# Optimization experiments

Hardware: AMD Instinct MI355X
Metric: run time of the kernel (lower is better)

Reference implementation:

```python
import jax, jax.numpy as jnp
import numpy as np

NUM_GRAPHS = 256


def _mean_aggregate(h, src, dst, num_nodes):
    # DGL copy_src + mean reduce: dst node gets mean of src-node features over in-edges.
    summed = jax.ops.segment_sum(h[src], dst, num_segments=num_nodes)  # [N, F]
    deg = jax.ops.segment_sum(jnp.ones((src.shape[0],), h.dtype), dst, num_segments=num_nodes)
    return summed / jnp.maximum(deg, 1.0)[:, None]


def setup_inputs() -> dict:
    key = jax.random.key(0)
    ks = jax.random.split(key, 10)
    N, E, D_IN, H1, H2, OUT = 50000, 800000, 128, 256, 128, 1
    s = lambda fan: 1.0 / np.sqrt(fan)
    return {
        "h": jax.random.normal(ks[0], (N, D_IN), jnp.float32),
        "src": jax.random.randint(ks[1], (E,), 0, N),
        "dst": jax.random.randint(ks[2], (E,), 0, N),
        "graph_ids": jnp.sort(jax.random.randint(ks[3], (N,), 0, NUM_GRAPHS)),
        "W1": jax.random.normal(ks[4], (D_IN, H1), jnp.float32) * s(D_IN),
        "b1": jnp.zeros((H1,), jnp.float32),
        "W2": jax.random.normal(ks[5], (H1, H1), jnp.float32) * s(H1),
        "b2": jnp.zeros((H1,), jnp.float32),
        "Wr1": jax.random.normal(ks[6], (H1, H2), jnp.float32) * s(H1),
        "br1": jnp.zeros((H2,), jnp.float32),
        "Wr2": jax.random.normal(ks[7], (H2, OUT), jnp.float32) * s(H2),
        "br2": jnp.zeros((OUT,), jnp.float32),
    }


def reference(h, src, dst, graph_ids, W1, b1, W2, b2, Wr1, br1, Wr2, br2):
    N = h.shape[0]
    # GCN layer 1: mean-aggregate then linear+ReLU
    h = _mean_aggregate(h, src, dst, N)
    h = jax.nn.relu(h @ W1 + b1)
    # GCN layer 2
    h = _mean_aggregate(h, src, dst, N)
    h = jax.nn.relu(h @ W2 + b2)
    # dgl.mean_nodes readout: per-graph mean of node features
    gsum = jax.ops.segment_sum(h, graph_ids, num_segments=NUM_GRAPHS)  # [G, H1]
    gcnt = jax.ops.segment_sum(jnp.ones((N,), h.dtype), graph_ids, num_segments=NUM_GRAPHS)
    hg = gsum / jnp.maximum(gcnt, 1.0)[:, None]
    hidden = hg @ Wr1 + br1
    return hidden @ Wr2 + br2  # [G, 1]
```

## Files before the change

kernel.cpp:

```cpp
#include <hip/hip_runtime.h>


#define NUM_GRAPHS 256

#define CNT_B0 0
#define CNT_NB 1024
#define CST_B0 (CNT_B0 + CNT_NB)
#define CST_NB 512
#define GST_B0 (CST_B0 + CST_NB)
#define GST_NB 64
#define WT1_B0 (GST_B0 + GST_NB)
#define WT1_NB 16
#define WT2_B0 (WT1_B0 + WT1_NB)
#define WT2_NB 32
#define MISC_NB (WT2_B0 + WT2_NB)

typedef __attribute__((ext_vector_type(8))) short bf16x8;
typedef __attribute__((ext_vector_type(4))) float f32x4;

__device__ inline unsigned short f2bf(float f) {
    unsigned u = __float_as_uint(f);
    return (unsigned short)((u + 0x7fff + ((u >> 16) & 1)) >> 16);
}
__device__ inline float bflo(unsigned u) { return __uint_as_float(u << 16); }
__device__ inline float bfhi(unsigned u) { return __uint_as_float(u & 0xffff0000u); }


__launch_bounds__(256)
__global__ void misc_kernel(const int* __restrict__ dst, const int* __restrict__ gids,
                            const float* __restrict__ h,
                            const float* __restrict__ W1, const float* __restrict__ W2,
                            int* __restrict__ cnt, unsigned short* __restrict__ rank,
                            int* __restrict__ gstart,
                            unsigned short* __restrict__ hb,
                            unsigned short* __restrict__ Wt1, unsigned short* __restrict__ Wt2,
                            int N, int E) {
    int b = blockIdx.x, tid = threadIdx.x;
    if (b < CST_B0) {
        int lid = (b - CNT_B0) * 256 + tid;
        for (int e = lid; e < E; e += CNT_NB * 256) {
            int d = __builtin_nontemporal_load(&dst[e]);
            int r = atomicAdd(&cnt[d], 1);
            __builtin_nontemporal_store((unsigned short)r, &rank[e]);
        }
    } else if (b < GST_B0) {
        int lid = (b - CST_B0) * 256 + tid;
        int total4 = N * 32;
        for (int i = lid; i < total4; i += CST_NB * 256) {
            float4 v = *(const float4*)(h + (size_t)i * 4);
            ushort4 o;
            o.x = f2bf(v.x); o.y = f2bf(v.y); o.z = f2bf(v.z); o.w = f2bf(v.w);
            *(ushort4*)(hb + (size_t)i * 4) = o;
        }
    } else if (b < WT1_B0) {
        int lid = (b - GST_B0) * 256 + tid;
        for (int n = lid; n < N; n += GST_NB * 256) {
            int g = gids[n];
            int gp = (n == 0) ? -1 : gids[n - 1];
            for (int x = gp + 1; x <= g; ++x) gstart[x] = n;
            if (n == N - 1)
                for (int x = g + 1; x <= NUM_GRAPHS; ++x) gstart[x] = N;
        }
    } else if (b < WT2_B0) {
        int lid = (b - WT1_B0) * 256 + tid;
        for (int i = lid; i < 256 * 128; i += WT1_NB * 256)
            Wt1[i] = f2bf(W1[(size_t)(i & 127) * 256 + (i >> 7)]);
    } else {
        int lid = (b - WT2_B0) * 256 + tid;
        for (int i = lid; i < 256 * 256; i += WT2_NB * 256)
            Wt2[i] = f2bf(W2[(size_t)(i & 255) * 256 + (i >> 8)]);
    }
}


__global__ void scan_kernel(const int* __restrict__ cnt, int* __restrict__ offs,
                            int* __restrict__ pval, int* __restrict__ pflag,
                            int N, int E) {
    __shared__ int wsum[16];
    __shared__ int sbase;
    int tid = threadIdx.x;
    int lane = tid & 63;
    int wid = tid >> 6;
    int b = blockIdx.x;
    int i = b * 1024 + tid;
    int v = (i < N) ? cnt[i] : 0;
    int x = v;
    #pragma unroll
    for (int d = 1; d < 64; d <<= 1) {
        int y = __shfl_up(x, d, 64);
        if (lane >= d) x += y;
    }
    if (lane == 63) wsum[wid] = x;
    __syncthreads();
    if (wid == 0) {
        int s = (lane < 16) ? wsum[lane] : 0;
        #pragma unroll
        for (int d = 1; d < 16; d <<= 1) {
            int y = __shfl_up(s, d, 64);
            if (lane >= d) s += y;
        }
        if (lane < 16) wsum[lane] = s;
    }
    __syncthreads();
    int wbase = (wid > 0) ? wsum[wid - 1] : 0;
    int ex = wbase + x - v;

    if (tid == 1023)
        atomicExch(&pval[b], (wbase + x) | 0x40000000);
    if (wid == 0) {
        int sum = 0;
        if (lane < b) {
            int pv;
            do { pv = atomicAdd(&pval[lane], 0); } while (!(pv & 0x40000000));
            sum = pv & 0x3fffffff;
        }
        #pragma unroll
        for (int d = 32; d > 0; d >>= 1) sum += __shfl_xor(sum, d, 64);
        if (lane == 0) sbase = sum;
    }
    __syncthreads();
    if (i < N) offs[i] = sbase + ex;
    if (b == 0 && tid == 0) offs[N] = E;
    (void)pflag;
}


__global__ void scatter_kernel(const int* __restrict__ src, const int* __restrict__ dst,
                               const int* __restrict__ offs,
                               const unsigned short* __restrict__ rank,
                               unsigned short* __restrict__ eidx, int E) {
    int e = blockIdx.x * blockDim.x + threadIdx.x;
    if (e < E) {
        int d = __builtin_nontemporal_load(&dst[e]);
        unsigned short r = __builtin_nontemporal_load(&rank[e]);
        int s = __builtin_nontemporal_load(&src[e]);
        eidx[offs[d] + (int)r] = (unsigned short)s;
    }
}


template <int D>
__global__ void agg_mean_bf16_kernel(const unsigned short* __restrict__ feat,
                                     const int* __restrict__ offs,
                                     const unsigned short* __restrict__ eidx,
                                     unsigned short* __restrict__ out, int N) {
    constexpr int VPL = D / 64;
    int wave = blockIdx.x * (blockDim.x >> 6) + (threadIdx.x >> 6);
    int lane = threadIdx.x & 63;
    if (wave >= N) return;
    int beg = offs[wave], end = offs[wave + 1];
    float acc[VPL];
    #pragma unroll
    for (int i = 0; i < VPL; ++i) acc[i] = 0.0f;

    for (int base = beg; base < end; base += 64) {
        int nchunk = end - base;
        if (nchunk > 64) nchunk = 64;
        int myIdx = (lane < nchunk) ? (int)eidx[base + lane] : 0;

        int j = 0;
        for (; j + 8 <= nchunk; j += 8) {
            int s[8];
            #pragma unroll
            for (int u = 0; u < 8; ++u) s[u] = __shfl(myIdx, j + u, 64);
            if constexpr (VPL == 2) {
                unsigned v[8];
                #pragma unroll
                for (int u = 0; u < 8; ++u)
                    v[u] = *(const unsigned*)(feat + (size_t)s[u] * D + lane * 2);
                #pragma unroll
                for (int u = 0; u < 8; ++u) { acc[0] += bflo(v[u]); acc[1] += bfhi(v[u]); }
            } else {
                uint2 v[8];
                #pragma unroll
                for (int u = 0; u < 8; ++u)
                    v[u] = *(const uint2*)(feat + (size_t)s[u] * D + lane * 4);
                #pragma unroll
                for (int u = 0; u < 8; ++u) {
                    acc[0] += bflo(v[u].x); acc[1] += bfhi(v[u].x);
                    acc[2] += bflo(v[u].y); acc[3] += bfhi(v[u].y);
                }
            }
        }
        for (; j < nchunk; ++j) {
            int s = __shfl(myIdx, j, 64);
            if constexpr (VPL == 2) {
                unsigned v = *(const unsigned*)(feat + (size_t)s * D + lane * 2);
                acc[0] += bflo(v); acc[1] += bfhi(v);
            } else {
                uint2 v = *(const uint2*)(feat + (size_t)s * D + lane * 4);
                acc[0] += bflo(v.x); acc[1] += bfhi(v.x);
                acc[2] += bflo(v.y); acc[3] += bfhi(v.y);
            }
        }
    }

    int deg = end - beg;
    float invd = 1.0f / (float)(deg > 0 ? deg : 1);
    unsigned short* orow = out + (size_t)wave * D + lane * VPL;
    if constexpr (VPL == 2) {
        ushort2 o; o.x = f2bf(acc[0] * invd); o.y = f2bf(acc[1] * invd);
        *(ushort2*)orow = o;
    } else {
        ushort4 o;
        o.x = f2bf(acc[0] * invd); o.y = f2bf(acc[1] * invd);
        o.z = f2bf(acc[2] * invd); o.w = f2bf(acc[3] * invd);
        *(ushort4*)orow = o;
    }
}


template <int K, int MODE>
__launch_bounds__(256)
__global__ void gemm_mfma_kernel(const unsigned short* __restrict__ A,
                                 const unsigned short* __restrict__ Wt,
                                 const float* __restrict__ bias,
                                 unsigned short* __restrict__ Cb,
                                 const int* __restrict__ gids,
                                 float* __restrict__ gsum,
                                 int N) {
    constexpr int LDS = 40;
    __shared__ unsigned short As[64 * LDS];
    __shared__ unsigned short Bs[256 * LDS];

    int tid = threadIdx.x;
    int wave = tid >> 6;
    int lane = tid & 63;
    int m = lane & 15;
    int q = lane >> 4;
    int rowBase = blockIdx.x * 64;

    f32x4 acc[4][4] = {};

    for (int kc = 0; kc < K; kc += 32) {
        {
            int r = tid >> 2;
            int seg = tid & 3;
            int gr = rowBase + r;
            uint4 v = make_uint4(0, 0, 0, 0);
            if (gr < N) v = *(const uint4*)(A + (size_t)gr * K + kc + seg * 8);
            *(uint4*)&As[r * LDS + seg * 8] = v;
        }
        #pragma unroll
        for (int it = 0; it < 4; ++it) {
            int n = (tid >> 2) + it * 64;
            int seg = tid & 3;
            uint4 v = *(const uint4*)(Wt + (size_t)n * K + kc + seg * 8);
            *(uint4*)&Bs[n * LDS + seg * 8] = v;
        }
        __syncthreads();

        bf16x8 af[4], bfr[4];
        #pragma unroll
        for (int r = 0; r < 4; ++r)
            af[r] = *(const bf16x8*)&As[(r * 16 + m) * LDS + q * 8];
        #pragma unroll
        for (int c = 0; c < 4; ++c)
            bfr[c] = *(const bf16x8*)&Bs[(wave * 64 + c * 16 + m) * LDS + q * 8];
        #pragma unroll
        for (int r = 0; r < 4; ++r)
            #pragma unroll
            for (int c = 0; c < 4; ++c)
                acc[r][c] = __builtin_amdgcn_mfma_f32_16x16x32_bf16(af[r], bfr[c], acc[r][c], 0, 0, 0);
        __syncthreads();
    }

    if constexpr (MODE == 0) {
        #pragma unroll
        for (int c = 0; c < 4; ++c) {
            int col = wave * 64 + c * 16 + m;
            float bv = bias[col];
            #pragma unroll
            for (int r = 0; r < 4; ++r) {
                #pragma unroll
                for (int reg = 0; reg < 4; ++reg) {
                    int grow = rowBase + r * 16 + q * 4 + reg;
                    if (grow < N)
                        Cb[(size_t)grow * 256 + col] = f2bf(fmaxf(acc[r][c][reg] + bv, 0.0f));
                }
            }
        }
    } else {
        int* sgid = (int*)As;
        if (tid < 64) {
            int gr = rowBase + tid;
            sgid[tid] = (gr < N) ? gids[gr] : 0x7fffffff;
        }
        __syncthreads();
        int lastValid = N - 1 - rowBase;
        if (lastValid > 63) lastValid = 63;
        int gmin = sgid[0];
        int gmax = sgid[lastValid];
        #pragma unroll
        for (int c = 0; c < 4; ++c) {
            int col = wave * 64 + c * 16 + m;
            float bv = bias[col];
            for (int g = gmin; g <= gmax; ++g) {
                float p = 0.0f;
                #pragma unroll
                for (int r = 0; r < 4; ++r) {
                    #pragma unroll
                    for (int reg = 0; reg < 4; ++reg) {
                        int lr = r * 16 + q * 4 + reg;
                        if (sgid[lr] == g)
                            p += fmaxf(acc[r][c][reg] + bv, 0.0f);
                    }
                }
                p += __shfl_xor(p, 16, 64);
                p += __shfl_xor(p, 32, 64);
                if (q == 0 && p != 0.0f)
                    atomicAdd(&gsum[g * 256 + col], p);
            }
        }
    }
}


__global__ void final_kernel(const float* __restrict__ gsum, const int* __restrict__ gstart,
                             const float* __restrict__ Wr1, const float* __restrict__ br1,
                             const float* __restrict__ Wr2, const float* __restrict__ br2,
                             float* __restrict__ out) {
    __shared__ float part[512];
    __shared__ float ws2[2];
    int g = blockIdx.x;
    int t = threadIdx.x;
    int j = t & 127;
    int kq = t >> 7;
    int c = gstart[g + 1] - gstart[g];
    float invc = 1.0f / (float)(c > 0 ? c : 1);
    const float* gs = gsum + g * 256;
    float acc = 0.0f;
    #pragma unroll 8
    for (int k = kq * 64; k < kq * 64 + 64; ++k)
        acc += gs[k] * Wr1[k * 128 + j];
    part[t] = acc;
    __syncthreads();
    if (t < 128) {
        float s = part[j] + part[128 + j] + part[256 + j] + part[384 + j];
        float p = (s * invc + br1[j]) * Wr2[j];
        #pragma unroll
        for (int d = 32; d > 0; d >>= 1) p += __shfl_down(p, d, 64);
        if ((t & 63) == 0) ws2[t >> 6] = p;
    }
    __syncthreads();
    if (t == 0) out[g] = ws2[0] + ws2[1] + br2[0];
}


extern "C" void kernel_launch(void* const* d_in, const int* in_sizes, int n_in,
                              void* d_out, int out_size, void* d_ws, size_t ws_size,
                              hipStream_t stream) {
    const float* h    = (const float*)d_in[0];
    const int*   src  = (const int*)d_in[1];
    const int*   dst  = (const int*)d_in[2];
    const int*   gids = (const int*)d_in[3];
    const float* W1   = (const float*)d_in[4];
    const float* b1   = (const float*)d_in[5];
    const float* W2   = (const float*)d_in[6];
    const float* b2   = (const float*)d_in[7];
    const float* Wr1  = (const float*)d_in[8];
    const float* br1  = (const float*)d_in[9];
    const float* Wr2  = (const float*)d_in[10];
    const float* br2  = (const float*)d_in[11];

    int N = in_sizes[0] / 128;
    int E = in_sizes[1];
    int nScanBlocks = (N + 1023) / 1024;

    char* w = (char*)d_ws;
    unsigned short* hb     = (unsigned short*)w;  w += (size_t)N * 128 * sizeof(unsigned short);
    unsigned short* h1b    = (unsigned short*)w;  w += (size_t)N * 256 * sizeof(unsigned short);
    unsigned short* aggOut = (unsigned short*)w;  w += (size_t)N * 256 * sizeof(unsigned short);
    int* cnt    = (int*)w;              w += (size_t)N * sizeof(int);
    float* gsum = (float*)w;            w += (size_t)NUM_GRAPHS * 256 * sizeof(float);
    int* pflag  = (int*)w;              w += 64 * sizeof(int);
    int* pval   = (int*)w;              w += 64 * sizeof(int);
    int* offs   = (int*)w;              w += (size_t)(N + 1) * sizeof(int);
    unsigned short* eidx = (unsigned short*)w;  w += (size_t)E * sizeof(unsigned short);
    unsigned short* rank = (unsigned short*)w;  w += (size_t)E * sizeof(unsigned short);
    unsigned short* Wt1 = (unsigned short*)w;   w += 256 * 128 * sizeof(unsigned short);
    unsigned short* Wt2 = (unsigned short*)w;   w += 256 * 256 * sizeof(unsigned short);
    int* gstart = (int*)w;              w += (size_t)(NUM_GRAPHS + 1) * sizeof(int);

    hipMemsetAsync(cnt, 0,
                   (size_t)N * sizeof(int) + (size_t)NUM_GRAPHS * 256 * sizeof(float) +
                   128 * sizeof(int),
                   stream);
    misc_kernel<<<MISC_NB, 256, 0, stream>>>(dst, gids, h, W1, W2, cnt, rank, gstart,
                                             hb, Wt1, Wt2, N, E);
    scan_kernel<<<nScanBlocks, 1024, 0, stream>>>(cnt, offs, pval, pflag, N, E);
    scatter_kernel<<<(E + 255) / 256, 256, 0, stream>>>(src, dst, offs, rank, eidx, E);

    agg_mean_bf16_kernel<128><<<(N + 3) / 4, 256, 0, stream>>>(hb, offs, eidx, aggOut, N);
    gemm_mfma_kernel<128, 0><<<(N + 63) / 64, 256, 0, stream>>>(aggOut, Wt1, b1, h1b, nullptr, nullptr, N);

    agg_mean_bf16_kernel<256><<<(N + 3) / 4, 256, 0, stream>>>(h1b, offs, eidx, aggOut, N);
    gemm_mfma_kernel<256, 1><<<(N + 63) / 64, 256, 0, stream>>>(aggOut, Wt2, b2, nullptr, gids, gsum, N);

    final_kernel<<<NUM_GRAPHS, 512, 0, stream>>>(gsum, gstart, Wr1, br1, Wr2, br2, (float*)d_out);
}
```

Measured before the change: 288.5 us.

## Split each wave across multiple edges with 16-byte feature loads in mean aggregation

The aggregation kernel now has each lane load 8 bf16 values (uint4) and splits the wave into sub-groups, each handling a different edge's row at once (4 edges per step for D=128, 2 for D=256). Partial sums are combined with xor shuffles at the end and only the first sub-group writes the output row. The intent is wider per-lane loads and more independent gathers in flight per wave, which cuts instruction count and raises memory-level parallelism for the random-row gather. Costs are extra cross-lane reductions, more registers per lane, a more complex remainder path, and a nontemporal hint on the edge-index load.

Result: slower. 598.9 us (+107.6%).

```diff
diff --git a/kernel.cpp b/kernel.cpp
--- a/kernel.cpp
+++ b/kernel.cpp
@@ -140,72 +140,86 @@
 
 
 template <int D>
+__launch_bounds__(256, 8)
 __global__ void agg_mean_bf16_kernel(const unsigned short* __restrict__ feat,
                                      const int* __restrict__ offs,
                                      const unsigned short* __restrict__ eidx,
                                      unsigned short* __restrict__ out, int N) {
-    constexpr int VPL = D / 64;
+    constexpr int LPR = D / 8;
+    constexpr int EPI = 64 / LPR;
     int wave = blockIdx.x * (blockDim.x >> 6) + (threadIdx.x >> 6);
     int lane = threadIdx.x & 63;
     if (wave >= N) return;
     int beg = offs[wave], end = offs[wave + 1];
-    float acc[VPL];
-    #pragma unroll
-    for (int i = 0; i < VPL; ++i) acc[i] = 0.0f;
+    int sub = lane / LPR;
+    int sl = lane % LPR;
+    const size_t rowOff = (size_t)sl * 8;
+
+    float acc[8] = {};
 
     for (int base = beg; base < end; base += 64) {
         int nchunk = end - base;
         if (nchunk > 64) nchunk = 64;
-        int myIdx = (lane < nchunk) ? (int)eidx[base + lane] : 0;
+        int myIdx = (lane < nchunk) ? (int)__builtin_nontemporal_load(&eidx[base + lane]) : 0;
 
         int j = 0;
-        for (; j + 8 <= nchunk; j += 8) {
-            int s[8];
-            #pragma unroll
-            for (int u = 0; u < 8; ++u) s[u] = __shfl(myIdx, j + u, 64);
-            if constexpr (VPL == 2) {
-                unsigned v[8];
-                #pragma unroll
-                for (int u = 0; u < 8; ++u)
-                    v[u] = *(const unsigned*)(feat + (size_t)s[u] * D + lane * 2);
-                #pragma unroll
-                for (int u = 0; u < 8; ++u) { acc[0] += bflo(v[u]); acc[1] += bfhi(v[u]); }
-            } else {
-                uint2 v[8];
-                #pragma unroll
-                for (int u = 0; u < 8; ++u)
-                    v[u] = *(const uint2*)(feat + (size_t)s[u] * D + lane * 4);
-                #pragma unroll
-                for (int u = 0; u < 8; ++u) {
-                    acc[0] += bflo(v[u].x); acc[1] += bfhi(v[u].x);
-                    acc[2] += bflo(v[u].y); acc[3] += bfhi(v[u].y);
+        for (; j + 8 * EPI <= nchunk; j += 8 * EPI) {
+            uint4 v[8];
+            #pragma unroll
+            for (int i = 0; i < 8; ++i) {
+                int s = __shfl(myIdx, j + i * EPI + sub, 64);
+                v[i] = *(const uint4*)(feat + (size_t)s * D + rowOff);
+            }
+            #pragma unroll
+            for (int i = 0; i < 8; ++i) {
+                acc[0] += bflo(v[i].x); acc[1] += bfhi(v[i].x);
+                acc[2] += bflo(v[i].y); acc[3] += bfhi(v[i].y);
+                acc[4] += bflo(v[i].z); acc[5] += bfhi(v[i].z);
+                acc[6] += bflo(v[i].w); acc[7] += bfhi(v[i].w);
+            }
+        }
+        int rem = nchunk - j;
+        if (rem > 0) {
+            uint4 v[8];
+            #pragma unroll
+            for (int i = 0; i < 8; ++i) {
+                if (i * EPI < rem) {
+                    int e = j + i * EPI + sub;
+                    int cl = (e < nchunk) ? e : (nchunk - 1);
+                    int s = __shfl(myIdx, cl, 64);
+                    v[i] = *(const uint4*)(feat + (size_t)s * D + rowOff);
                 }
             }
-        }
-        for (; j < nchunk; ++j) {
-            int s = __shfl(myIdx, j, 64);
-            if constexpr (VPL == 2) {
-                unsigned v = *(const unsigned*)(feat + (size_t)s * D + lane * 2);
-                acc[0] += bflo(v); acc[1] += bfhi(v);
-            } else {
-                uint2 v = *(const uint2*)(feat + (size_t)s * D + lane * 4);
-                acc[0] += bflo(v.x); acc[1] += bfhi(v.x);
-                acc[2] += bflo(v.y); acc[3] += bfhi(v.y);
-            }
-        }
+            #pragma unroll
+            for (int i = 0; i < 8; ++i) {
+                if (i * EPI < rem) {
+                    int e = j + i * EPI + sub;
+                    if (e < nchunk) {
+                        acc[0] += bflo(v[i].x); acc[1] += bfhi(v[i].x);
+                        acc[2] += bflo(v[i].y); acc[3] += bfhi(v[i].y);
+                        acc[4] += bflo(v[i].z); acc[5] += bfhi(v[i].z);
+                        acc[6] += bflo(v[i].w); acc[7] += bfhi(v[i].w);
+                    }
+                }
+            }
+        }
+    }
+
+    #pragma unroll
+    for (int k = 0; k < 8; ++k) {
+        if constexpr (EPI == 4) acc[k] += __shfl_xor(acc[k], 16, 64);
+        acc[k] += __shfl_xor(acc[k], 32, 64);
     }
 
     int deg = end - beg;
     float invd = 1.0f / (float)(deg > 0 ? deg : 1);
-    unsigned short* orow = out + (size_t)wave * D + lane * VPL;
-    if constexpr (VPL == 2) {
-        ushort2 o; o.x = f2bf(acc[0] * invd); o.y = f2bf(acc[1] * invd);
-        *(ushort2*)orow = o;
-    } else {
-        ushort4 o;
-        o.x = f2bf(acc[0] * invd); o.y = f2bf(acc[1] * invd);
-        o.z = f2bf(acc[2] * invd); o.w = f2bf(acc[3] * invd);
-        *(ushort4*)orow = o;
+    if (lane < LPR) {
+        uint4 o;
+        o.x = (unsigned)f2bf(acc[0] * invd) | ((unsigned)f2bf(acc[1] * invd) << 16);
+        o.y = (unsigned)f2bf(acc[2] * invd) | ((unsigned)f2bf(acc[3] * invd) << 16);
+        o.z = (unsigned)f2bf(acc[4] * invd) | ((unsigned)f2bf(acc[5] * invd) << 16);
+        o.w = (unsigned)f2bf(acc[6] * invd) | ((unsigned)f2bf(acc[7] * invd) << 16);
+        *(uint4*)(out + (size_t)wave * D + rowOff) = o;
     }
 }
 
```
